# Optimization experiments

Measured on AMD Instinct MI355X. Metric: run time of the kernel, lower is better.

The kernel has to match this reference:

```python
import jax, jax.numpy as jnp
import numpy as np

N, E = 50000, 1600000
FEAT, HID, HEADS = 256, 64, 2
NEG_SLOPE = 0.2


def gat_conv(x, src, dst, W, att_src, att_dst, bias, heads, out_ch):
    """PyG GATConv (concat=True, self-loops already appended to src/dst)."""
    n = x.shape[0]
    h = (x @ W).reshape(n, heads, out_ch)                      # [N,H,C]
    a_src = jnp.einsum('nhc,hc->nh', h, att_src)               # [N,H]
    a_dst = jnp.einsum('nhc,hc->nh', h, att_dst)               # [N,H]
    alpha = jax.nn.leaky_relu(a_src[src] + a_dst[dst], NEG_SLOPE)  # [E',H]
    # segment softmax over incoming edges of each dst node
    amax = jax.ops.segment_max(alpha, dst, num_segments=n)
    alpha = jnp.exp(alpha - amax[dst])
    denom = jax.ops.segment_sum(alpha, dst, num_segments=n)
    alpha = alpha / (denom[dst] + 1e-16)
    msg = h[src] * alpha[..., None]                            # [E',H,C]
    out = jax.ops.segment_sum(msg, dst, num_segments=n)        # [N,H,C]
    return out.reshape(n, heads * out_ch) + bias


def setup_inputs() -> dict:
    key = jax.random.key(0)
    ks = jax.random.split(key, 10)
    x = jax.random.normal(ks[0], (N, FEAT), dtype=jnp.float32)
    edge_index = jax.random.randint(ks[1], (2, E), 0, N, dtype=jnp.int64)
    s1 = 1.0 / np.sqrt(FEAT)
    s2 = 1.0 / np.sqrt(HID * HEADS)
    sa = 1.0 / np.sqrt(HID)
    return {
        'x': x,
        'edge_index': edge_index,
        'W1': jax.random.uniform(ks[2], (FEAT, HEADS * HID), jnp.float32, -s1, s1),
        'att_src1': jax.random.uniform(ks[3], (HEADS, HID), jnp.float32, -sa, sa),
        'att_dst1': jax.random.uniform(ks[4], (HEADS, HID), jnp.float32, -sa, sa),
        'b1': jnp.zeros((HEADS * HID,), jnp.float32),
        'W2': jax.random.uniform(ks[5], (HEADS * HID, HID), jnp.float32, -s2, s2),
        'att_src2': jax.random.uniform(ks[6], (1, HID), jnp.float32, -sa, sa),
        'att_dst2': jax.random.uniform(ks[7], (1, HID), jnp.float32, -sa, sa),
        'b2': jnp.zeros((HID,), jnp.float32),
    }


def reference(x, edge_index, W1, att_src1, att_dst1, b1, W2, att_src2, att_dst2, b2):
    n = x.shape[0]
    loop = jnp.arange(n, dtype=edge_index.dtype)
    src = jnp.concatenate([edge_index[0], loop])   # add self loops (PyG default)
    dst = jnp.concatenate([edge_index[1], loop])
    h = gat_conv(x, src, dst, W1, att_src1, att_dst1, b1, HEADS, HID)
    h = jax.nn.relu(h)  # dropout is identity in eval mode
    h = gat_conv(h, src, dst, W2, att_src2, att_dst2, b2, 1, HID)
    return jax.nn.log_softmax(h, axis=1)
```

## Files before the change

kernel.cpp:

```cpp
#include <hip/hip_runtime.h>
#include <hip/hip_bf16.h>
#include <math.h>

typedef short bf16x8 __attribute__((ext_vector_type(8)));
typedef float f32x4 __attribute__((ext_vector_type(4)));

#define BSHIFT 7
#define BWIDTH 128
#define PCHUNK 4096

__global__ void prep_kernel(int* __restrict__ bcnt,
                            const float* __restrict__ W1, const float* __restrict__ W2,
                            __hip_bfloat16* __restrict__ W1t,
                            __hip_bfloat16* __restrict__ W2t) {
    if (blockIdx.x == 0) {
        bcnt[threadIdx.x] = 0;
        bcnt[threadIdx.x + 256] = 0;
        return;
    }
    int idx = (blockIdx.x - 1) * 256 + threadIdx.x;
    const int n1 = 128 * 256;
    if (idx < n1) {
        int nn = idx >> 8, kk = idx & 255;
        W1t[idx] = __float2bfloat16(W1[kk * 128 + nn]);
    } else {
        int j = idx - n1;
        if (j < 64 * 128) {
            int nn = j >> 7, kk = j & 127;
            W2t[j] = __float2bfloat16(W2[kk * 64 + nn]);
        }
    }
}

__global__ __launch_bounds__(256) void bucket_hist(const int* __restrict__ ei, int E,
                                                   int* __restrict__ bcnt) {
    __shared__ int h[512];
    int tid = threadIdx.x;
    for (int i = tid; i < 512; i += 256) h[i] = 0;
    __syncthreads();
    int start = blockIdx.x * PCHUNK;
    int cnt = min(PCHUNK, E - start);
    for (int i = tid; i < cnt; i += 256)
        atomicAdd(&h[ei[E + start + i] >> BSHIFT], 1);
    __syncthreads();
    for (int i = tid; i < 512; i += 256)
        if (h[i]) atomicAdd(&bcnt[i], h[i]);
}

__global__ __launch_bounds__(512) void bucket_scan(const int* __restrict__ bcnt,
                                                   int* __restrict__ bbase,
                                                   int* __restrict__ bcur,
                                                   int nbk, int n) {
    __shared__ int s[512];
    int tid = threadIdx.x;
    int nodes = 0;
    if (tid < nbk) nodes = min(BWIDTH, n - (tid << BSHIFT));
    int v = (tid < nbk) ? bcnt[tid] + nodes : 0;
    s[tid] = v;
    __syncthreads();
    #pragma unroll
    for (int o = 1; o < 512; o <<= 1) {
        int t = (tid >= o) ? s[tid - o] : 0;
        __syncthreads();
        s[tid] += t;
        __syncthreads();
    }
    if (tid < nbk) {
        int ex = s[tid] - v;
        bbase[tid] = ex;
        bcur[tid] = ex - (tid << BSHIFT);
    }
    if (tid == nbk) bbase[nbk] = s[tid];
}

__global__ __launch_bounds__(256) void partition_edges(const int* __restrict__ ei, int E,
                                                       int* __restrict__ bcur,
                                                       int* __restrict__ tmp) {
    __shared__ int2 stage[PCHUNK];
    __shared__ int h[512];
    __shared__ int lbase[512];
    int tid = threadIdx.x;
    int start = blockIdx.x * PCHUNK;
    int cnt = min(PCHUNK, E - start);
    for (int i = tid; i < 512; i += 256) h[i] = 0;
    __syncthreads();
    for (int i = tid; i < cnt; i += 256) {
        int s = ei[start + i];
        int d = ei[E + start + i];
        stage[i] = make_int2(s, d);
        atomicAdd(&h[d >> BSHIFT], 1);
    }
    __syncthreads();
    for (int i = tid; i < 512; i += 256) {
        if (h[i] > 0) lbase[i] = atomicAdd(&bcur[i], h[i]);
        h[i] = 0;
    }
    __syncthreads();
    for (int i = tid; i < cnt; i += 256) {
        int2 e = stage[i];
        int b = e.y >> BSHIFT;
        int r = atomicAdd(&h[b], 1);
        tmp[lbase[b] + r] = (e.x << BSHIFT) | (e.y & (BWIDTH - 1));
    }
}

__global__ __launch_bounds__(256) void bucket_csr(const int* __restrict__ bbase,
                                                  const int* __restrict__ tmp,
                                                  int* __restrict__ offs,
                                                  int* __restrict__ srcs,
                                                  int n, int nbk) {
    __shared__ int cnt[BWIDTH];
    __shared__ int sa[BWIDTH];
    __shared__ int cur[BWIDTH];
    int b = blockIdx.x;
    int tid = threadIdx.x;
    int node0 = b << BSHIFT;
    int nnodes = min(BWIDTH, n - node0);
    int cb = bbase[b];
    int ce = bbase[b + 1];
    int tb = cb - node0;
    int ecnt = (ce - cb) - nnodes;

    if (tid < BWIDTH) cnt[tid] = (tid < nnodes) ? 1 : 0;
    __syncthreads();
    for (int i = tid; i < ecnt; i += 256)
        atomicAdd(&cnt[tmp[tb + i] & (BWIDTH - 1)], 1);
    __syncthreads();
    if (tid < BWIDTH) sa[tid] = cnt[tid];
    __syncthreads();
    #pragma unroll
    for (int o = 1; o < BWIDTH; o <<= 1) {
        int v = 0;
        if (tid < BWIDTH) { v = sa[tid]; if (tid >= o) v += sa[tid - o]; }
        __syncthreads();
        if (tid < BWIDTH) sa[tid] = v;
        __syncthreads();
    }
    if (tid < BWIDTH) {
        int ex = sa[tid] - cnt[tid];
        if (tid < nnodes) {
            offs[node0 + tid] = cb + ex;
            srcs[cb + ex] = node0 + tid;
        }
        cur[tid] = ex + (tid < nnodes ? 1 : 0);
    }
    if (b == nbk - 1 && tid == 0) offs[n] = ce;
    __syncthreads();
    for (int i = tid; i < ecnt; i += 256) {
        int e = tmp[tb + i];
        int li = e & (BWIDTH - 1);
        int r = atomicAdd(&cur[li], 1);
        srcs[cb + r] = e >> BSHIFT;
    }
}

template <bool A_BF16, int NT, int HEADS, int KSTEPS>
__global__ __launch_bounds__(256) void gemm_att(
    const void* __restrict__ Av, const __hip_bfloat16* __restrict__ Bt,
    __hip_bfloat16* __restrict__ C,
    const float* __restrict__ atts, const float* __restrict__ attd,
    float* __restrict__ a_s, float* __restrict__ a_d, int M) {
    constexpr int K = KSTEPS * 32;
    constexpr int N = NT * 16;
    constexpr int KH = 128;
    constexpr int NCH = (K + KH - 1) / KH;
    constexpr int LDB = KH + 8;
    __shared__ __hip_bfloat16 Bs[N][LDB];

    int tid = threadIdx.x;
    int w = tid >> 6, l = tid & 63;
    int q = l >> 4, m16 = l & 15;
    int bm = blockIdx.x * 64;
    int arow = bm + w * 16 + m16;
    if (arow >= M) arow = M - 1;

    f32x4 acc[NT];
    #pragma unroll
    for (int t = 0; t < NT; t++) acc[t] = (f32x4){0.f, 0.f, 0.f, 0.f};

    #pragma unroll
    for (int ch = 0; ch < NCH; ch++) {
        const int cb = ch * KH;
        bf16x8 af[4];
        float4 st[8];
        if (A_BF16) {
            const __hip_bfloat16* A = (const __hip_bfloat16*)Av + (size_t)arow * K + cb + q * 8;
            #pragma unroll
            for (int t = 0; t < 4; t++)
                af[t] = *(const bf16x8*)(A + t * 32);
        } else {
            const float* A = (const float*)Av + (size_t)arow * K + cb + q * 8;
            #pragma unroll
            for (int t = 0; t < 4; t++) {
                st[2 * t]     = *(const float4*)(A + t * 32);
                st[2 * t + 1] = *(const float4*)(A + t * 32 + 4);
            }
        }
        for (int i = tid; i < (N * KH) / 8; i += 256) {
            int row = i >> 4;
            int k = (i & 15) * 8;
            *(uint4*)&Bs[row][k] = *(const uint4*)(Bt + (size_t)row * K + cb + k);
        }
        __syncthreads();
        if (!A_BF16) {
            #pragma unroll
            for (int t = 0; t < 4; t++) {
                union { __hip_bfloat16 h[8]; bf16x8 v; } u;
                float4 v0 = st[2 * t], v1 = st[2 * t + 1];
                u.h[0] = __float2bfloat16(v0.x); u.h[1] = __float2bfloat16(v0.y);
                u.h[2] = __float2bfloat16(v0.z); u.h[3] = __float2bfloat16(v0.w);
                u.h[4] = __float2bfloat16(v1.x); u.h[5] = __float2bfloat16(v1.y);
                u.h[6] = __float2bfloat16(v1.z); u.h[7] = __float2bfloat16(v1.w);
                af[t] = u.v;
            }
        }
        #pragma unroll
        for (int t = 0; t < 4; t++) {
            #pragma unroll
            for (int c = 0; c < NT; c++) {
                bf16x8 b = *(const bf16x8*)&Bs[c * 16 + m16][t * 32 + q * 8];
                acc[c] = __builtin_amdgcn_mfma_f32_16x16x32_bf16(af[t], b, acc[c], 0, 0, 0);
            }
        }
        if (ch + 1 < NCH) __syncthreads();
    }

    #pragma unroll
    for (int t = 0; t < NT; t++) {
        #pragma unroll
        for (int r = 0; r < 4; r++) {
            int row = bm + w * 16 + q * 4 + r;
            if (row < M) C[(size_t)row * N + t * 16 + m16] = __float2bfloat16(acc[t][r]);
        }
    }

    float ps[HEADS][4], pd[HEADS][4];
    #pragma unroll
    for (int hh = 0; hh < HEADS; hh++)
        #pragma unroll
        for (int r = 0; r < 4; r++) { ps[hh][r] = 0.f; pd[hh][r] = 0.f; }
    #pragma unroll
    for (int t = 0; t < NT; t++) {
        int ch = t * 16 + m16;
        float asw = atts[ch], adw = attd[ch];
        int hh = (HEADS == 2) ? (t >> 2) : 0;
        #pragma unroll
        for (int r = 0; r < 4; r++) {
            ps[hh][r] = fmaf(acc[t][r], asw, ps[hh][r]);
            pd[hh][r] = fmaf(acc[t][r], adw, pd[hh][r]);
        }
    }
    #pragma unroll
    for (int o = 1; o < 16; o <<= 1) {
        #pragma unroll
        for (int hh = 0; hh < HEADS; hh++)
            #pragma unroll
            for (int r = 0; r < 4; r++) {
                ps[hh][r] += __shfl_xor(ps[hh][r], o);
                pd[hh][r] += __shfl_xor(pd[hh][r], o);
            }
    }
    if (m16 == 0) {
        #pragma unroll
        for (int r = 0; r < 4; r++) {
            int row = bm + w * 16 + q * 4 + r;
            if (row < M) {
                if (HEADS == 2) {
                    a_s[row * 2]     = ps[0][r];
                    a_s[row * 2 + 1] = ps[1][r];
                    a_d[row * 2]     = pd[0][r];
                    a_d[row * 2 + 1] = pd[1][r];
                } else {
                    a_s[row] = ps[0][r];
                    a_d[row] = pd[0][r];
                }
            }
        }
    }
}

__device__ __forceinline__ float leaky(float r) {
    return r < 0.f ? 0.2f * r : r;
}

__device__ __forceinline__ void unpack2(unsigned u, float& lo, float& hi) {
    lo = __uint_as_float(u << 16);
    hi = __uint_as_float(u & 0xffff0000u);
}

__global__ __launch_bounds__(256) void edge_agg_l1(
    const int* __restrict__ offs, const int* __restrict__ srcs,
    const __hip_bfloat16* __restrict__ h1, const float* __restrict__ asv,
    const float* __restrict__ adv, const float* __restrict__ bias,
    __hip_bfloat16* __restrict__ out, int n) {
    int d = (blockIdx.x * blockDim.x + threadIdx.x) >> 6;
    int lane = threadIdx.x & 63;
    if (d >= n) return;
    int start = offs[d], end = offs[d + 1];
    int cnt = end - start;
    int sub = lane & 15;
    int g = lane >> 4;
    int ch0 = sub * 8;
    int hsel = sub >> 3;
    float ad = adv[2 * d + hsel];

    float wsum = 0.f;
    float acc[8];
    #pragma unroll
    for (int k = 0; k < 8; k++) acc[k] = 0.f;

    int full = cnt >> 2;
    int ib = start + g;
    int jj = 0;
    int pA = 0, pB = 0, pC = 0, pD = 0;
    if (jj + 4 <= full) {
        pA = srcs[ib];      pB = srcs[ib + 4];
        pC = srcs[ib + 8];  pD = srcs[ib + 12];
    }
    for (; jj + 4 <= full; jj += 4) {
        int sA = pA, sB = pB, sC = pC, sD = pD;
        if (jj + 8 <= full) {
            int nb = ib + (jj + 4) * 4;
            pA = srcs[nb];      pB = srcs[nb + 4];
            pC = srcs[nb + 8];  pD = srcs[nb + 12];
        }
        uint4 vA = *(const uint4*)(h1 + (size_t)sA * 128 + ch0);
        uint4 vB = *(const uint4*)(h1 + (size_t)sB * 128 + ch0);
        uint4 vC = *(const uint4*)(h1 + (size_t)sC * 128 + ch0);
        uint4 vD = *(const uint4*)(h1 + (size_t)sD * 128 + ch0);
        float aA = asv[2 * sA + hsel];
        float aB = asv[2 * sB + hsel];
        float aC = asv[2 * sC + hsel];
        float aD = asv[2 * sD + hsel];
        float wA = __expf(leaky(aA + ad));
        float wB = __expf(leaky(aB + ad));
        float wC = __expf(leaky(aC + ad));
        float wD = __expf(leaky(aD + ad));
        wsum += (wA + wB) + (wC + wD);
        float f0, f1, f2, f3, f4, f5, f6, f7;
        unpack2(vA.x, f0, f1); unpack2(vA.y, f2, f3);
        unpack2(vA.z, f4, f5); unpack2(vA.w, f6, f7);
        acc[0] = fmaf(wA, f0, acc[0]); acc[1] = fmaf(wA, f1, acc[1]);
        acc[2] = fmaf(wA, f2, acc[2]); acc[3] = fmaf(wA, f3, acc[3]);
        acc[4] = fmaf(wA, f4, acc[4]); acc[5] = fmaf(wA, f5, acc[5]);
        acc[6] = fmaf(wA, f6, acc[6]); acc[7] = fmaf(wA, f7, acc[7]);
        unpack2(vB.x, f0, f1); unpack2(vB.y, f2, f3);
        unpack2(vB.z, f4, f5); unpack2(vB.w, f6, f7);
        acc[0] = fmaf(wB, f0, acc[0]); acc[1] = fmaf(wB, f1, acc[1]);
        acc[2] = fmaf(wB, f2, acc[2]); acc[3] = fmaf(wB, f3, acc[3]);
        acc[4] = fmaf(wB, f4, acc[4]); acc[5] = fmaf(wB, f5, acc[5]);
        acc[6] = fmaf(wB, f6, acc[6]); acc[7] = fmaf(wB, f7, acc[7]);
        unpack2(vC.x, f0, f1); unpack2(vC.y, f2, f3);
        unpack2(vC.z, f4, f5); unpack2(vC.w, f6, f7);
        acc[0] = fmaf(wC, f0, acc[0]); acc[1] = fmaf(wC, f1, acc[1]);
        acc[2] = fmaf(wC, f2, acc[2]); acc[3] = fmaf(wC, f3, acc[3]);
        acc[4] = fmaf(wC, f4, acc[4]); acc[5] = fmaf(wC, f5, acc[5]);
        acc[6] = fmaf(wC, f6, acc[6]); acc[7] = fmaf(wC, f7, acc[7]);
        unpack2(vD.x, f0, f1); unpack2(vD.y, f2, f3);
        unpack2(vD.z, f4, f5); unpack2(vD.w, f6, f7);
        acc[0] = fmaf(wD, f0, acc[0]); acc[1] = fmaf(wD, f1, acc[1]);
        acc[2] = fmaf(wD, f2, acc[2]); acc[3] = fmaf(wD, f3, acc[3]);
        acc[4] = fmaf(wD, f4, acc[4]); acc[5] = fmaf(wD, f5, acc[5]);
        acc[6] = fmaf(wD, f6, acc[6]); acc[7] = fmaf(wD, f7, acc[7]);
    }
    for (; jj < full; jj++) {
        int s = srcs[ib + jj * 4];
        uint4 v = *(const uint4*)(h1 + (size_t)s * 128 + ch0);
        float a = asv[2 * s + hsel];
        float wA = __expf(leaky(a + ad));
        wsum += wA;
        float f0, f1, f2, f3, f4, f5, f6, f7;
        unpack2(v.x, f0, f1); unpack2(v.y, f2, f3);
        unpack2(v.z, f4, f5); unpack2(v.w, f6, f7);
        acc[0] = fmaf(wA, f0, acc[0]); acc[1] = fmaf(wA, f1, acc[1]);
        acc[2] = fmaf(wA, f2, acc[2]); acc[3] = fmaf(wA, f3, acc[3]);
        acc[4] = fmaf(wA, f4, acc[4]); acc[5] = fmaf(wA, f5, acc[5]);
        acc[6] = fmaf(wA, f6, acc[6]); acc[7] = fmaf(wA, f7, acc[7]);
    }
    if (full * 4 + g < cnt) {
        int s = srcs[ib + full * 4];
        uint4 v = *(const uint4*)(h1 + (size_t)s * 128 + ch0);
        float a = asv[2 * s + hsel];
        float wA = __expf(leaky(a + ad));
        wsum += wA;
        float f0, f1, f2, f3, f4, f5, f6, f7;
        unpack2(v.x, f0, f1); unpack2(v.y, f2, f3);
        unpack2(v.z, f4, f5); unpack2(v.w, f6, f7);
        acc[0] = fmaf(wA, f0, acc[0]); acc[1] = fmaf(wA, f1, acc[1]);
        acc[2] = fmaf(wA, f2, acc[2]); acc[3] = fmaf(wA, f3, acc[3]);
        acc[4] = fmaf(wA, f4, acc[4]); acc[5] = fmaf(wA, f5, acc[5]);
        acc[6] = fmaf(wA, f6, acc[6]); acc[7] = fmaf(wA, f7, acc[7]);
    }
    #pragma unroll
    for (int o = 16; o < 64; o <<= 1) {
        #pragma unroll
        for (int k = 0; k < 8; k++) acc[k] += __shfl_xor(acc[k], o);
        wsum += __shfl_xor(wsum, o);
    }

    if (lane < 16) {
        float invh = 1.f / (wsum + 1e-16f);
        float4 b0 = *(const float4*)(bias + ch0);
        float4 b1 = *(const float4*)(bias + ch0 + 4);
        union { __hip_bfloat16 h[8]; uint4 u; } o2;
        o2.h[0] = __float2bfloat16(fmaxf(fmaf(acc[0], invh, b0.x), 0.f));
        o2.h[1] = __float2bfloat16(fmaxf(fmaf(acc[1], invh, b0.y), 0.f));
        o2.h[2] = __float2bfloat16(fmaxf(fmaf(acc[2], invh, b0.z), 0.f));
        o2.h[3] = __float2bfloat16(fmaxf(fmaf(acc[3], invh, b0.w), 0.f));
        o2.h[4] = __float2bfloat16(fmaxf(fmaf(acc[4], invh, b1.x), 0.f));
        o2.h[5] = __float2bfloat16(fmaxf(fmaf(acc[5], invh, b1.y), 0.f));
        o2.h[6] = __float2bfloat16(fmaxf(fmaf(acc[6], invh, b1.z), 0.f));
        o2.h[7] = __float2bfloat16(fmaxf(fmaf(acc[7], invh, b1.w), 0.f));
        *(uint4*)(out + (size_t)d * 128 + ch0) = o2.u;
    }
}

__global__ __launch_bounds__(256) void edge_agg_l2(
    const int* __restrict__ offs, const int* __restrict__ srcs,
    const __hip_bfloat16* __restrict__ h2, const float* __restrict__ asv,
    const float* __restrict__ adv, const float* __restrict__ bias,
    float* __restrict__ out, int n) {
    int d = (blockIdx.x * blockDim.x + threadIdx.x) >> 6;
    int lane = threadIdx.x & 63;
    if (d >= n) return;
    int start = offs[d], end = offs[d + 1];
    int cnt = end - start;
    int sub = lane & 7;
    int g = lane >> 3;
    int ch0 = sub * 8;
    float ad = adv[d];

    float wsum = 0.f;
    float acc[8];
    #pragma unroll
    for (int k = 0; k < 8; k++) acc[k] = 0.f;

    int full = cnt >> 3;
    int ib = start + g;
    int jj = 0;
    int pA = 0, pB = 0, pC = 0, pD = 0;
    if (jj + 4 <= full) {
        pA = srcs[ib];       pB = srcs[ib + 8];
        pC = srcs[ib + 16];  pD = srcs[ib + 24];
    }
    for (; jj + 4 <= full; jj += 4) {
        int sA = pA, sB = pB, sC = pC, sD = pD;
        if (jj + 8 <= full) {
            int nb = ib + (jj + 4) * 8;
            pA = srcs[nb];       pB = srcs[nb + 8];
            pC = srcs[nb + 16];  pD = srcs[nb + 24];
        }
        uint4 vA = *(const uint4*)(h2 + (size_t)sA * 64 + ch0);
        uint4 vB = *(const uint4*)(h2 + (size_t)sB * 64 + ch0);
        uint4 vC = *(const uint4*)(h2 + (size_t)sC * 64 + ch0);
        uint4 vD = *(const uint4*)(h2 + (size_t)sD * 64 + ch0);
        float aA = asv[sA], aB = asv[sB], aC = asv[sC], aD = asv[sD];
        float wA = __expf(leaky(aA + ad));
        float wB = __expf(leaky(aB + ad));
        float wC = __expf(leaky(aC + ad));
        float wD = __expf(leaky(aD + ad));
        wsum += (wA + wB) + (wC + wD);
        float f0, f1, f2, f3, f4, f5, f6, f7;
        unpack2(vA.x, f0, f1); unpack2(vA.y, f2, f3);
        unpack2(vA.z, f4, f5); unpack2(vA.w, f6, f7);
        acc[0] = fmaf(wA, f0, acc[0]); acc[1] = fmaf(wA, f1, acc[1]);
        acc[2] = fmaf(wA, f2, acc[2]); acc[3] = fmaf(wA, f3, acc[3]);
        acc[4] = fmaf(wA, f4, acc[4]); acc[5] = fmaf(wA, f5, acc[5]);
        acc[6] = fmaf(wA, f6, acc[6]); acc[7] = fmaf(wA, f7, acc[7]);
        unpack2(vB.x, f0, f1); unpack2(vB.y, f2, f3);
        unpack2(vB.z, f4, f5); unpack2(vB.w, f6, f7);
        acc[0] = fmaf(wB, f0, acc[0]); acc[1] = fmaf(wB, f1, acc[1]);
        acc[2] = fmaf(wB, f2, acc[2]); acc[3] = fmaf(wB, f3, acc[3]);
        acc[4] = fmaf(wB, f4, acc[4]); acc[5] = fmaf(wB, f5, acc[5]);
        acc[6] = fmaf(wB, f6, acc[6]); acc[7] = fmaf(wB, f7, acc[7]);
        unpack2(vC.x, f0, f1); unpack2(vC.y, f2, f3);
        unpack2(vC.z, f4, f5); unpack2(vC.w, f6, f7);
        acc[0] = fmaf(wC, f0, acc[0]); acc[1] = fmaf(wC, f1, acc[1]);
        acc[2] = fmaf(wC, f2, acc[2]); acc[3] = fmaf(wC, f3, acc[3]);
        acc[4] = fmaf(wC, f4, acc[4]); acc[5] = fmaf(wC, f5, acc[5]);
        acc[6] = fmaf(wC, f6, acc[6]); acc[7] = fmaf(wC, f7, acc[7]);
        unpack2(vD.x, f0, f1); unpack2(vD.y, f2, f3);
        unpack2(vD.z, f4, f5); unpack2(vD.w, f6, f7);
        acc[0] = fmaf(wD, f0, acc[0]); acc[1] = fmaf(wD, f1, acc[1]);
        acc[2] = fmaf(wD, f2, acc[2]); acc[3] = fmaf(wD, f3, acc[3]);
        acc[4] = fmaf(wD, f4, acc[4]); acc[5] = fmaf(wD, f5, acc[5]);
        acc[6] = fmaf(wD, f6, acc[6]); acc[7] = fmaf(wD, f7, acc[7]);
    }
    for (; jj < full; jj++) {
        int s = srcs[ib + jj * 8];
        uint4 v = *(const uint4*)(h2 + (size_t)s * 64 + ch0);
        float a = asv[s];
        float wA = __expf(leaky(a + ad));
        wsum += wA;
        float f0, f1, f2, f3, f4, f5, f6, f7;
        unpack2(v.x, f0, f1); unpack2(v.y, f2, f3);
        unpack2(v.z, f4, f5); unpack2(v.w, f6, f7);
        acc[0] = fmaf(wA, f0, acc[0]); acc[1] = fmaf(wA, f1, acc[1]);
        acc[2] = fmaf(wA, f2, acc[2]); acc[3] = fmaf(wA, f3, acc[3]);
        acc[4] = fmaf(wA, f4, acc[4]); acc[5] = fmaf(wA, f5, acc[5]);
        acc[6] = fmaf(wA, f6, acc[6]); acc[7] = fmaf(wA, f7, acc[7]);
    }
    if (full * 8 + g < cnt) {
        int s = srcs[ib + full * 8];
        uint4 v = *(const uint4*)(h2 + (size_t)s * 64 + ch0);
        float a = asv[s];
        float wA = __expf(leaky(a + ad));
        wsum += wA;
        float f0, f1, f2, f3, f4, f5, f6, f7;
        unpack2(v.x, f0, f1); unpack2(v.y, f2, f3);
        unpack2(v.z, f4, f5); unpack2(v.w, f6, f7);
        acc[0] = fmaf(wA, f0, acc[0]); acc[1] = fmaf(wA, f1, acc[1]);
        acc[2] = fmaf(wA, f2, acc[2]); acc[3] = fmaf(wA, f3, acc[3]);
        acc[4] = fmaf(wA, f4, acc[4]); acc[5] = fmaf(wA, f5, acc[5]);
        acc[6] = fmaf(wA, f6, acc[6]); acc[7] = fmaf(wA, f7, acc[7]);
    }
    #pragma unroll
    for (int o = 8; o < 64; o <<= 1) {
        #pragma unroll
        for (int k = 0; k < 8; k++) acc[k] += __shfl_xor(acc[k], o);
        wsum += __shfl_xor(wsum, o);
    }

    float inv = 1.f / (wsum + 1e-16f);
    float4 b0 = *(const float4*)(bias + ch0);
    float4 b1 = *(const float4*)(bias + ch0 + 4);
    float v[8];
    v[0] = fmaf(acc[0], inv, b0.x); v[1] = fmaf(acc[1], inv, b0.y);
    v[2] = fmaf(acc[2], inv, b0.z); v[3] = fmaf(acc[3], inv, b0.w);
    v[4] = fmaf(acc[4], inv, b1.x); v[5] = fmaf(acc[5], inv, b1.y);
    v[6] = fmaf(acc[6], inv, b1.z); v[7] = fmaf(acc[7], inv, b1.w);

    float vm = v[0];
    #pragma unroll
    for (int k = 1; k < 8; k++) vm = fmaxf(vm, v[k]);
    #pragma unroll
    for (int o = 1; o < 8; o <<= 1) vm = fmaxf(vm, __shfl_xor(vm, o));
    float se_loc = 0.f;
    #pragma unroll
    for (int k = 0; k < 8; k++) se_loc += __expf(v[k] - vm);
    #pragma unroll
    for (int o = 1; o < 8; o <<= 1) se_loc += __shfl_xor(se_loc, o);
    float lse = vm + logf(se_loc);

    if (lane < 8) {
        float4 o0 = make_float4(v[0] - lse, v[1] - lse, v[2] - lse, v[3] - lse);
        float4 o1 = make_float4(v[4] - lse, v[5] - lse, v[6] - lse, v[7] - lse);
        *(float4*)(out + (size_t)d * 64 + ch0) = o0;
        *(float4*)(out + (size_t)d * 64 + ch0 + 4) = o1;
    }
}

extern "C" void kernel_launch(void* const* d_in, const int* in_sizes, int n_in,
                              void* d_out, int out_size, void* d_ws, size_t ws_size,
                              hipStream_t stream) {
    const float* x    = (const float*)d_in[0];
    const int*   ei   = (const int*)d_in[1];
    const float* W1   = (const float*)d_in[2];
    const float* as1w = (const float*)d_in[3];
    const float* ad1w = (const float*)d_in[4];
    const float* b1   = (const float*)d_in[5];
    const float* W2   = (const float*)d_in[6];
    const float* as2w = (const float*)d_in[7];
    const float* ad2w = (const float*)d_in[8];
    const float* b2   = (const float*)d_in[9];
    float* out = (float*)d_out;

    const int n = in_sizes[0] / 256;
    const int E = in_sizes[1] / 2;
    const int tot = E + n;
    const int nbk = (n + BWIDTH - 1) / BWIDTH;

    char* p = (char*)d_ws;
    auto alloc = [&](size_t bytes) {
        void* r = (void*)p;
        p += (bytes + 255) & ~(size_t)255;
        return r;
    };
    int*   offs  = (int*)alloc((size_t)(n + 1) * 4);
    int*   srcs  = (int*)alloc((size_t)tot * 4);
    int*   tmp   = (int*)alloc((size_t)E * 4);
    int*   bcnt  = (int*)alloc(512 * 4);
    int*   bbase = (int*)alloc(512 * 4);
    int*   bcur  = (int*)alloc(512 * 4);
    __hip_bfloat16* W1t = (__hip_bfloat16*)alloc((size_t)128 * 256 * 2);
    __hip_bfloat16* W2t = (__hip_bfloat16*)alloc((size_t)64 * 128 * 2);
    __hip_bfloat16* h1  = (__hip_bfloat16*)alloc((size_t)n * 128 * 2);
    __hip_bfloat16* out1= (__hip_bfloat16*)alloc((size_t)n * 128 * 2);
    __hip_bfloat16* h2  = (__hip_bfloat16*)alloc((size_t)n * 64 * 2);
    float* a_s1 = (float*)alloc((size_t)n * 2 * 4);
    float* a_d1 = (float*)alloc((size_t)n * 2 * 4);
    float* a_s2 = (float*)alloc((size_t)n * 4);
    float* a_d2 = (float*)alloc((size_t)n * 4);

    int pblocks = (E + PCHUNK - 1) / PCHUNK;

    prep_kernel<<<1 + (128 * 256 + 64 * 128 + 255) / 256, 256, 0, stream>>>(
        bcnt, W1, W2, W1t, W2t);

    bucket_hist<<<pblocks, 256, 0, stream>>>(ei, E, bcnt);
    bucket_scan<<<1, 512, 0, stream>>>(bcnt, bbase, bcur, nbk, n);
    partition_edges<<<pblocks, 256, 0, stream>>>(ei, E, bcur, tmp);
    bucket_csr<<<nbk, 256, 0, stream>>>(bbase, tmp, offs, srcs, n, nbk);

    gemm_att<false, 8, 2, 8><<<(n + 63) / 64, 256, 0, stream>>>(
        x, W1t, h1, as1w, ad1w, a_s1, a_d1, n);
    edge_agg_l1<<<((size_t)n * 64 + 255) / 256, 256, 0, stream>>>(
        offs, srcs, h1, a_s1, a_d1, b1, out1, n);

    gemm_att<true, 4, 1, 4><<<(n + 63) / 64, 256, 0, stream>>>(
        out1, W2t, h2, as2w, ad2w, a_s2, a_d2, n);
    edge_agg_l2<<<((size_t)n * 64 + 255) / 256, 256, 0, stream>>>(
        offs, srcs, h2, a_s2, a_d2, b2, out, n);
}
```

Measured before the change: 267.1 us.

## Precompute per-edge attention weights into packed edge records for aggregation

The CSR build now runs after the first GEMM and writes 16-byte per-edge records holding a byte offset into h1, both heads' exp(leaky) weights, and the dst id. A new kernel builds 8-byte records for layer 2 with precomputed weights. The aggregation kernels then skip the random a_src gathers and the exp work in their inner loops. In exchange the edge-list traffic grows from 4 to 16 and 8 bytes per edge, and there is an extra kernel pass. Because the weights are no longer max-subtracted, exp could overflow, though the earlier code already computed them the same way.

```diff
diff --git a/kernel.cpp b/kernel.cpp
--- a/kernel.cpp
+++ b/kernel.cpp
@@ -104,14 +104,21 @@
     }
 }
 
+__device__ __forceinline__ float leaky(float r) {
+    return r < 0.f ? 0.2f * r : r;
+}
+
 __global__ __launch_bounds__(256) void bucket_csr(const int* __restrict__ bbase,
                                                   const int* __restrict__ tmp,
                                                   int* __restrict__ offs,
-                                                  int* __restrict__ srcs,
+                                                  uint4* __restrict__ rec1,
+                                                  const float* __restrict__ asv1,
+                                                  const float* __restrict__ adv1,
                                                   int n, int nbk) {
     __shared__ int cnt[BWIDTH];
     __shared__ int sa[BWIDTH];
     __shared__ int cur[BWIDTH];
+    __shared__ float adl[2 * BWIDTH];
     int b = blockIdx.x;
     int tid = threadIdx.x;
     int node0 = b << BSHIFT;
@@ -122,6 +129,7 @@
     int ecnt = (ce - cb) - nnodes;
 
     if (tid < BWIDTH) cnt[tid] = (tid < nnodes) ? 1 : 0;
+    if (tid < 2 * nnodes) adl[tid] = adv1[2 * node0 + tid];
     __syncthreads();
     for (int i = tid; i < ecnt; i += 256)
         atomicAdd(&cnt[tmp[tb + i] & (BWIDTH - 1)], 1);
@@ -139,8 +147,14 @@
     if (tid < BWIDTH) {
         int ex = sa[tid] - cnt[tid];
         if (tid < nnodes) {
-            offs[node0 + tid] = cb + ex;
-            srcs[cb + ex] = node0 + tid;
+            int dst = node0 + tid;
+            offs[dst] = cb + ex;
+            float2 a = *(const float2*)(asv1 + 2 * dst);
+            float w0 = __expf(leaky(a.x + adl[2 * tid]));
+            float w1 = __expf(leaky(a.y + adl[2 * tid + 1]));
+            rec1[cb + ex] = make_uint4((unsigned)dst * 256u,
+                                       __float_as_uint(w0), __float_as_uint(w1),
+                                       (unsigned)dst);
         }
         cur[tid] = ex + (tid < nnodes ? 1 : 0);
     }
@@ -150,8 +164,27 @@
         int e = tmp[tb + i];
         int li = e & (BWIDTH - 1);
         int r = atomicAdd(&cur[li], 1);
-        srcs[cb + r] = e >> BSHIFT;
-    }
+        int src = e >> BSHIFT;
+        int dst = node0 + li;
+        float2 a = *(const float2*)(asv1 + 2 * src);
+        float w0 = __expf(leaky(a.x + adl[2 * li]));
+        float w1 = __expf(leaky(a.y + adl[2 * li + 1]));
+        rec1[cb + r] = make_uint4((unsigned)src * 256u,
+                                  __float_as_uint(w0), __float_as_uint(w1),
+                                  (unsigned)dst);
+    }
+}
+
+__global__ __launch_bounds__(256) void build_rec2(
+    const uint4* __restrict__ rec1, const float* __restrict__ asv2,
+    const float* __restrict__ adv2, uint2* __restrict__ rec2, int tot) {
+    int i = blockIdx.x * blockDim.x + threadIdx.x;
+    if (i >= tot) return;
+    uint4 r = rec1[i];
+    int src = (int)(r.x >> 8);
+    int dst = (int)r.w;
+    float w = __expf(leaky(asv2[src] + adv2[dst]));
+    rec2[i] = make_uint2(r.x >> 1, __float_as_uint(w));
 }
 
 template <bool A_BF16, int NT, int HEADS, int KSTEPS>
@@ -279,19 +312,14 @@
     }
 }
 
-__device__ __forceinline__ float leaky(float r) {
-    return r < 0.f ? 0.2f * r : r;
-}
-
 __device__ __forceinline__ void unpack2(unsigned u, float& lo, float& hi) {
     lo = __uint_as_float(u << 16);
     hi = __uint_as_float(u & 0xffff0000u);
 }
 
 __global__ __launch_bounds__(256) void edge_agg_l1(
-    const int* __restrict__ offs, const int* __restrict__ srcs,
-    const __hip_bfloat16* __restrict__ h1, const float* __restrict__ asv,
-    const float* __restrict__ adv, const float* __restrict__ bias,
+    const int* __restrict__ offs, const uint4* __restrict__ rec1,
+    const __hip_bfloat16* __restrict__ h1, const float* __restrict__ bias,
     __hip_bfloat16* __restrict__ out, int n) {
     int d = (blockIdx.x * blockDim.x + threadIdx.x) >> 6;
     int lane = threadIdx.x & 63;
@@ -300,9 +328,9 @@
     int cnt = end - start;
     int sub = lane & 15;
     int g = lane >> 4;
-    int ch0 = sub * 8;
+    unsigned cboff = (unsigned)(sub * 8) * 2u;
     int hsel = sub >> 3;
-    float ad = adv[2 * d + hsel];
+    const char* hb = (const char*)h1;
 
     float wsum = 0.f;
     float acc[8];
@@ -312,30 +340,26 @@
     int full = cnt >> 2;
     int ib = start + g;
     int jj = 0;
-    int pA = 0, pB = 0, pC = 0, pD = 0;
+    uint4 pA, pB, pC, pD;
     if (jj + 4 <= full) {
-        pA = srcs[ib];      pB = srcs[ib + 4];
-        pC = srcs[ib + 8];  pD = srcs[ib + 12];
+        pA = rec1[ib];      pB = rec1[ib + 4];
+        pC = rec1[ib + 8];  pD = rec1[ib + 12];
     }
     for (; jj + 4 <= full; jj += 4) {
-        int sA = pA, sB = pB, sC = pC, sD = pD;
+        uint4 rA = pA, rB = pB, rC = pC, rD = pD;
         if (jj + 8 <= full) {
             int nb = ib + (jj + 4) * 4;
-            pA = srcs[nb];      pB = srcs[nb + 4];
-            pC = srcs[nb + 8];  pD = srcs[nb + 12];
-        }
-        uint4 vA = *(const uint4*)(h1 + (size_t)sA * 128 + ch0);
-        uint4 vB = *(const uint4*)(h1 + (size_t)sB * 128 + ch0);
-        uint4 vC = *(const uint4*)(h1 + (size_t)sC * 128 + ch0);
-        uint4 vD = *(const uint4*)(h1 + (size_t)sD * 128 + ch0);
-        float aA = asv[2 * sA + hsel];
-        float aB = asv[2 * sB + hsel];
-        float aC = asv[2 * sC + hsel];
-        float aD = asv[2 * sD + hsel];
-        float wA = __expf(leaky(aA + ad));
-        float wB = __expf(leaky(aB + ad));
-        float wC = __expf(leaky(aC + ad));
-        float wD = __expf(leaky(aD + ad));
+            pA = rec1[nb];      pB = rec1[nb + 4];
+            pC = rec1[nb + 8];  pD = rec1[nb + 12];
+        }
+        uint4 vA = *(const uint4*)(hb + (rA.x + cboff));
+        uint4 vB = *(const uint4*)(hb + (rB.x + cboff));
+        uint4 vC = *(const uint4*)(hb + (rC.x + cboff));
+        uint4 vD = *(const uint4*)(hb + (rD.x + cboff));
+        float wA = __uint_as_float(hsel ? rA.z : rA.y);
+        float wB = __uint_as_float(hsel ? rB.z : rB.y);
+        float wC = __uint_as_float(hsel ? rC.z : rC.y);
+        float wD = __uint_as_float(hsel ? rD.z : rD.y);
         wsum += (wA + wB) + (wC + wD);
         float f0, f1, f2, f3, f4, f5, f6, f7;
         unpack2(vA.x, f0, f1); unpack2(vA.y, f2, f3);
@@ -364,10 +388,9 @@
         acc[6] = fmaf(wD, f6, acc[6]); acc[7] = fmaf(wD, f7, acc[7]);
     }
     for (; jj < full; jj++) {
-        int s = srcs[ib + jj * 4];
-        uint4 v = *(const uint4*)(h1 + (size_t)s * 128 + ch0);
-        float a = asv[2 * s + hsel];
-        float wA = __expf(leaky(a + ad));
+        uint4 r = rec1[ib + jj * 4];
+        uint4 v = *(const uint4*)(hb + (r.x + cboff));
+        float wA = __uint_as_float(hsel ? r.z : r.y);
         wsum += wA;
         float f0, f1, f2, f3, f4, f5, f6, f7;
         unpack2(v.x, f0, f1); unpack2(v.y, f2, f3);
@@ -378,10 +401,9 @@
         acc[6] = fmaf(wA, f6, acc[6]); acc[7] = fmaf(wA, f7, acc[7]);
     }
     if (full * 4 + g < cnt) {
-        int s = srcs[ib + full * 4];
-        uint4 v = *(const uint4*)(h1 + (size_t)s * 128 + ch0);
-        float a = asv[2 * s + hsel];
-        float wA = __expf(leaky(a + ad));
+        uint4 r = rec1[ib + full * 4];
+        uint4 v = *(const uint4*)(hb + (r.x + cboff));
+        float wA = __uint_as_float(hsel ? r.z : r.y);
         wsum += wA;
         float f0, f1, f2, f3, f4, f5, f6, f7;
         unpack2(v.x, f0, f1); unpack2(v.y, f2, f3);
@@ -399,6 +421,7 @@
     }
 
     if (lane < 16) {
+        int ch0 = sub * 8;
         float invh = 1.f / (wsum + 1e-16f);
         float4 b0 = *(const float4*)(bias + ch0);
         float4 b1 = *(const float4*)(bias + ch0 + 4);
@@ -416,9 +439,8 @@
 }
 
 __global__ __launch_bounds__(256) void edge_agg_l2(
-    const int* __restrict__ offs, const int* __restrict__ srcs,
-    const __hip_bfloat16* __restrict__ h2, const float* __restrict__ asv,
-    const float* __restrict__ adv, const float* __restrict__ bias,
+    const int* __restrict__ offs, const uint2* __restrict__ rec2,
+    const __hip_bfloat16* __restrict__ h2, const float* __restrict__ bias,
     float* __restrict__ out, int n) {
     int d = (blockIdx.x * blockDim.x + threadIdx.x) >> 6;
     int lane = threadIdx.x & 63;
@@ -427,8 +449,8 @@
     int cnt = end - start;
     int sub = lane & 7;
     int g = lane >> 3;
-    int ch0 = sub * 8;
-    float ad = adv[d];
+    unsigned cboff = (unsigned)(sub * 8) * 2u;
+    const char* hb = (const char*)h2;
 
     float wsum = 0.f;
     float acc[8];
@@ -438,27 +460,26 @@
     int full = cnt >> 3;
     int ib = start + g;
     int jj = 0;
-    int pA = 0, pB = 0, pC = 0, pD = 0;
+    uint2 pA, pB, pC, pD;
     if (jj + 4 <= full) {
-        pA = srcs[ib];       pB = srcs[ib + 8];
-        pC = srcs[ib + 16];  pD = srcs[ib + 24];
+        pA = rec2[ib];       pB = rec2[ib + 8];
+        pC = rec2[ib + 16];  pD = rec2[ib + 24];
     }
     for (; jj + 4 <= full; jj += 4) {
-        int sA = pA, sB = pB, sC = pC, sD = pD;
+        uint2 rA = pA, rB = pB, rC = pC, rD = pD;
         if (jj + 8 <= full) {
             int nb = ib + (jj + 4) * 8;
-            pA = srcs[nb];       pB = srcs[nb + 8];
-            pC = srcs[nb + 16];  pD = srcs[nb + 24];
-        }
-        uint4 vA = *(const uint4*)(h2 + (size_t)sA * 64 + ch0);
-        uint4 vB = *(const uint4*)(h2 + (size_t)sB * 64 + ch0);
-        uint4 vC = *(const uint4*)(h2 + (size_t)sC * 64 + ch0);
-        uint4 vD = *(const uint4*)(h2 + (size_t)sD * 64 + ch0);
-        float aA = asv[sA], aB = asv[sB], aC = asv[sC], aD = asv[sD];
-        float wA = __expf(leaky(aA + ad));
-        float wB = __expf(leaky(aB + ad));
-        float wC = __expf(leaky(aC + ad));
-        float wD = __expf(leaky(aD + ad));
+            pA = rec2[nb];       pB = rec2[nb + 8];
+            pC = rec2[nb + 16];  pD = rec2[nb + 24];
+        }
+        uint4 vA = *(const uint4*)(hb + (rA.x + cboff));
+        uint4 vB = *(const uint4*)(hb + (rB.x + cboff));
+        uint4 vC = *(const uint4*)(hb + (rC.x + cboff));
+        uint4 vD = *(const uint4*)(hb + (rD.x + cboff));
+        float wA = __uint_as_float(rA.y);
+        float wB = __uint_as_float(rB.y);
+        float wC = __uint_as_float(rC.y);
+        float wD = __uint_as_float(rD.y);
         wsum += (wA + wB) + (wC + wD);
         float f0, f1, f2, f3, f4, f5, f6, f7;
         unpack2(vA.x, f0, f1); unpack2(vA.y, f2, f3);
@@ -487,10 +508,9 @@
         acc[6] = fmaf(wD, f6, acc[6]); acc[7] = fmaf(wD, f7, acc[7]);
     }
     for (; jj < full; jj++) {
-        int s = srcs[ib + jj * 8];
-        uint4 v = *(const uint4*)(h2 + (size_t)s * 64 + ch0);
-        float a = asv[s];
-        float wA = __expf(leaky(a + ad));
+        uint2 r = rec2[ib + jj * 8];
+        uint4 v = *(const uint4*)(hb + (r.x + cboff));
+        float wA = __uint_as_float(r.y);
         wsum += wA;
         float f0, f1, f2, f3, f4, f5, f6, f7;
         unpack2(v.x, f0, f1); unpack2(v.y, f2, f3);
@@ -501,10 +521,9 @@
         acc[6] = fmaf(wA, f6, acc[6]); acc[7] = fmaf(wA, f7, acc[7]);
     }
     if (full * 8 + g < cnt) {
-        int s = srcs[ib + full * 8];
-        uint4 v = *(const uint4*)(h2 + (size_t)s * 64 + ch0);
-        float a = asv[s];
-        float wA = __expf(leaky(a + ad));
+        uint2 r = rec2[ib + full * 8];
+        uint4 v = *(const uint4*)(hb + (r.x + cboff));
+        float wA = __uint_as_float(r.y);
         wsum += wA;
         float f0, f1, f2, f3, f4, f5, f6, f7;
         unpack2(v.x, f0, f1); unpack2(v.y, f2, f3);
@@ -521,6 +540,7 @@
         wsum += __shfl_xor(wsum, o);
     }
 
+    int ch0 = sub * 8;
     float inv = 1.f / (wsum + 1e-16f);
     float4 b0 = *(const float4*)(bias + ch0);
     float4 b1 = *(const float4*)(bias + ch0 + 4);
@@ -577,11 +597,12 @@
         return r;
     };
     int*   offs  = (int*)alloc((size_t)(n + 1) * 4);
-    int*   srcs  = (int*)alloc((size_t)tot * 4);
     int*   tmp   = (int*)alloc((size_t)E * 4);
     int*   bcnt  = (int*)alloc(512 * 4);
     int*   bbase = (int*)alloc(512 * 4);
     int*   bcur  = (int*)alloc(512 * 4);
+    uint4* rec1  = (uint4*)alloc((size_t)tot * 16);
+    uint2* rec2  = (uint2*)alloc((size_t)tot * 8);
     __hip_bfloat16* W1t = (__hip_bfloat16*)alloc((size_t)128 * 256 * 2);
     __hip_bfloat16* W2t = (__hip_bfloat16*)alloc((size_t)64 * 128 * 2);
     __hip_bfloat16* h1  = (__hip_bfloat16*)alloc((size_t)n * 128 * 2);
@@ -600,15 +621,18 @@
     bucket_hist<<<pblocks, 256, 0, stream>>>(ei, E, bcnt);
     bucket_scan<<<1, 512, 0, stream>>>(bcnt, bbase, bcur, nbk, n);
     partition_edges<<<pblocks, 256, 0, stream>>>(ei, E, bcur, tmp);
-    bucket_csr<<<nbk, 256, 0, stream>>>(bbase, tmp, offs, srcs, n, nbk);
 
     gemm_att<false, 8, 2, 8><<<(n + 63) / 64, 256, 0, stream>>>(
         x, W1t, h1, as1w, ad1w, a_s1, a_d1, n);
+
+    bucket_csr<<<nbk, 256, 0, stream>>>(bbase, tmp, offs, rec1, a_s1, a_d1, n, nbk);
+
     edge_agg_l1<<<((size_t)n * 64 + 255) / 256, 256, 0, stream>>>(
-        offs, srcs, h1, a_s1, a_d1, b1, out1, n);
+        offs, rec1, h1, b1, out1, n);
 
     gemm_att<true, 4, 1, 4><<<(n + 63) / 64, 256, 0, stream>>>(
         out1, W2t, h2, as2w, ad2w, a_s2, a_d2, n);
+    build_rec2<<<(tot + 255) / 256, 256, 0, stream>>>(rec1, a_s2, a_d2, rec2, tot);
     edge_agg_l2<<<((size_t)n * 64 + 255) / 256, 256, 0, stream>>>(
-        offs, srcs, h2, a_s2, a_d2, b2, out, n);
-}
+        offs, rec2, h2, b2, out, n);
+}
```

New measurement: 293.8 us. +10.0%, slower.
